# Performance work log

Measured on AMD Instinct MI355X. Metric: run time of the kernel, lower is better.

Reference implementation:

```python
import jax, jax.numpy as jnp
import numpy as np

B = 4      # cfg.TRAIN.IMS_PER_BATCH
P = 256    # proposals per image (equal per image; all labels > 0)
C = 151    # cfg.MODEL.NUM_CLASSES
R = 51     # cfg.MODEL.NUM_RELATIONS
W = 0.5    # cfg.REL_INFER.NONE_BGREL_WEIGHT


def setup_inputs() -> dict:
    key = jax.random.key(0)
    k1, k2, k3, k4 = jax.random.split(key, 4)
    roi_scores = jax.random.normal(k1, (B * P, C), dtype=jnp.float32)
    rel_scores = jax.random.normal(k2, (B * P * P, R), dtype=jnp.float32)
    roi_labels = jax.random.randint(k3, (B * P,), 1, C, dtype=jnp.int32)  # labels > 0 (fg only)
    # sparse relation co-occurrence matrix densified; background relation slice set to 1
    relationship_mat = (jax.random.uniform(k4, (C, C, R)) < 0.05).astype(jnp.float32)
    relationship_mat = relationship_mat.at[:, :, 0].set(1.0)
    return {
        "roi_scores": roi_scores,
        "rel_scores": rel_scores,
        "relationship_mat": relationship_mat,
        "roi_labels": roi_labels,
        "num_images": B,
    }


def reference(roi_scores, rel_scores, relationship_mat, roi_labels, num_images):
    nb = num_images
    p = roi_scores.shape[0] // nb
    rel = rel_scores.reshape(nb, p, p, -1)          # [B, P, P, R]
    labels = roi_labels.reshape(nb, p)              # [B, P]
    # computed in the original forward but unused by the returned loss
    _unary = jax.nn.log_softmax(roi_scores, axis=1)
    off_diag = (1.0 - jnp.eye(p, dtype=roi_scores.dtype))  # zero out p == q pairs

    def per_image(lab, rl):
        # lab: [P] int, rl: [P, P, R]
        A = relationship_mat[lab]        # [P, C, R]  rows gathered by subject label
        At = relationship_mat[:, lab]    # [C, P, R]  cols gathered by subject label
        # b[p,q,c] = A[p,c,0]*rl[p,q,0] + W * sum_{r>=1} A[p,c,r]*rl[p,q,r]
        b = A[:, None, :, 0] * rl[:, :, None, 0] \
            + W * jnp.einsum('pcr,pqr->pqc', A[..., 1:], rl[..., 1:])
        # t[p,q,c] = At[c,p,0]*rl[q,p,0] + W * sum_{r>=1} At[c,p,r]*rl[q,p,r]
        t = At[..., 0].T[:, None, :] * rl[..., 0].T[:, :, None] \
            + W * jnp.einsum('cpr,qpr->pqc', At[..., 1:], rl[..., 1:])
        theta = 0.5 * (b + t) * off_diag[:, :, None]  # mask diagonal pairs
        theta = theta.sum(0)                          # sum over partner p -> [P, C]
        logp = jax.nn.log_softmax(theta, axis=1)
        return -logp[jnp.arange(p), lab]              # [P]

    loss = jax.vmap(per_image)(labels, rel)           # [B, P]
    return loss.mean()
```

## Files before the change

kernel.cpp:

```cpp
#include <hip/hip_runtime.h>
#include <math.h>

#define NB 4
#define PP 256
#define CC 151
#define RR 51
#define CM 160
#define KS 64
#define NROW (NB*PP)
#define RELTOT (NB*PP*PP*RR)
#define ALIM (RELTOT - 8)
#define MLB 10240

typedef _Float16 half8 __attribute__((ext_vector_type(8)));
typedef float floatx16 __attribute__((ext_vector_type(16)));

#define OFF_M1 ((size_t)0)
#define OFF_M2 (OFF_M1 + (size_t)CC*MLB*2)
#define OFF_PT (OFF_M2 + (size_t)CC*MLB*2)

__global__ __launch_bounds__(256) void prep_kernel(const float* __restrict__ M,
                                                   _Float16* __restrict__ m1,
                                                   _Float16* __restrict__ m2,
                                                   float* __restrict__ out) {
    const int l = blockIdx.x;
    const int mat = blockIdx.y;
    if (l == 0 && mat == 0 && threadIdx.x == 0) *out = 0.f;
    _Float16* dst = (mat ? m2 : m1) + (size_t)l * MLB;
    for (int e = threadIdx.x; e < MLB; e += 256) {
        int oct = e / 1280;
        int rem = e - oct * 1280;
        int c = rem >> 3, j = rem & 7;
        int r = oct * 8 + j;
        float v = 0.f;
        if (r < RR && c < CC) {
            size_t src = ((size_t)(mat ? c * CC + l : l * CC + c)) * RR + r;
            v = (r == 0 ? 0.5f : 0.25f) * M[src];
        }
        dst[e] = (_Float16)v;
    }
}

__global__ __launch_bounds__(256, 2) void gemm_kernel(const float* __restrict__ rel,
                                                      const _Float16* __restrict__ m1,
                                                      const _Float16* __restrict__ m2,
                                                      const int* __restrict__ labels,
                                                      float* __restrict__ part) {
    const int tid  = threadIdx.x;
    const int ks   = blockIdx.x & 63;
    const int rbk  = (blockIdx.x >> 6) & 1;
    const int n    = blockIdx.x >> 7;
    const int wave = tid >> 6, lane = tid & 63;
    const int m32  = lane & 31, kh = lane >> 5;
    const int i0   = ks * 4;
    const int rowimg = rbk * 128 + wave * 32 + m32;

    int labs[4];
    #pragma unroll
    for (int j = 0; j < 4; ++j) labs[j] = labels[n * PP + i0 + j];

    floatx16 acc[5];
    #pragma unroll
    for (int ct = 0; ct < 5; ++ct)
        #pragma unroll
        for (int r2 = 0; r2 < 16; ++r2) acc[ct][r2] = 0.f;

    auto loadA = [&](int h, float* v) {
        const int il = h >> 3, mh = (h >> 2) & 1, t = h & 3;
        const int i = i0 + il;
        const int r0 = t * 16 + kh * 8;
        int idx = mh ? ((n * PP + rowimg) * PP + i) * RR + r0
                     : ((n * PP + i) * PP + rowimg) * RR + r0;
        idx = min(idx, ALIM);
        const float* p = rel + idx;
        #pragma unroll
        for (int j = 0; j < 8; ++j) v[j] = p[j];
    };
    auto loadB = [&](int h, half8* b) {
        const int il = h >> 3, mh = (h >> 2) & 1, t = h & 3;
        const _Float16* p = (mh ? m2 : m1) + (size_t)labs[il] * MLB + t * 2560
                          + (size_t)(kh * 160 + m32) * 8;
        #pragma unroll
        for (int ct = 0; ct < 5; ++ct) b[ct] = *(const half8*)(p + ct * 256);
    };
    auto computeStep = [&](int h, const float* av, const half8* bv) {
        const int il = h >> 3;
        const bool dz = (i0 + il) == rowimg;
        half8 a;
        #pragma unroll
        for (int j = 0; j < 8; ++j) a[j] = (_Float16)(dz ? 0.f : av[j]);
        #pragma unroll
        for (int ct = 0; ct < 5; ++ct)
            acc[ct] = __builtin_amdgcn_mfma_f32_32x32x16_f16(a, bv[ct], acc[ct], 0, 0, 0);
    };

    float aS[3][8];
    half8 bS[3][5];
    loadA(0, aS[0]); loadB(0, bS[0]);
    __builtin_amdgcn_sched_barrier(0);
    loadA(1, aS[1]); loadB(1, bS[1]);
    __builtin_amdgcn_sched_barrier(0);
    loadA(2, aS[2]); loadB(2, bS[2]);
    __builtin_amdgcn_sched_barrier(0);

    #pragma unroll
    for (int h = 0; h < 32; ++h) {
        computeStep(h, aS[h % 3], bS[h % 3]);
        if (h + 3 < 32) {
            loadA(h + 3, aS[(h + 3) % 3]);
            loadB(h + 3, bS[(h + 3) % 3]);
            __builtin_amdgcn_sched_barrier(0);
        }
    }

    float* pb = part + ((size_t)ks * NROW + n * PP + rbk * 128 + wave * 32) * CM;
    #pragma unroll
    for (int ct = 0; ct < 5; ++ct)
        #pragma unroll
        for (int reg = 0; reg < 16; ++reg) {
            int row = (reg & 3) + 8 * (reg >> 2) + 4 * kh;
            pb[(size_t)row * CM + ct * 32 + m32] = acc[ct][reg];
        }
}

__global__ __launch_bounds__(256) void reduce_loss_kernel(const float* __restrict__ part,
                                                          const int* __restrict__ labels,
                                                          float* __restrict__ out) {
    __shared__ float th[CM];
    const int row = blockIdx.x;
    const int t = threadIdx.x;
    if (t < CM) {
        float s = 0.f;
        #pragma unroll
        for (int ks = 0; ks < KS; ++ks)
            s += part[((size_t)ks * NROW + row) * CM + t];
        th[t] = s;
    }
    __syncthreads();
    if (t < 64) {
        float v0 = (t < CC)       ? th[t]       : -INFINITY;
        float v1 = (t + 64 < CC)  ? th[t + 64]  : -INFINITY;
        float v2 = (t + 128 < CC) ? th[t + 128] : -INFINITY;
        float m = fmaxf(v0, fmaxf(v1, v2));
        #pragma unroll
        for (int o = 32; o > 0; o >>= 1) m = fmaxf(m, __shfl_xor(m, o, 64));
        float s = 0.f;
        if (t < CC)       s += expf(v0 - m);
        if (t + 64 < CC)  s += expf(v1 - m);
        if (t + 128 < CC) s += expf(v2 - m);
        #pragma unroll
        for (int o = 32; o > 0; o >>= 1) s += __shfl_xor(s, o, 64);
        if (t == 0) {
            atomicAdd(out, (m + logf(s) - th[labels[row]]) * (1.0f / NROW));
        }
    }
}

extern "C" void kernel_launch(void* const* d_in, const int* in_sizes, int n_in,
                              void* d_out, int out_size, void* d_ws, size_t ws_size,
                              hipStream_t stream) {
    const float* rel    = (const float*)d_in[1];
    const float* relmat = (const float*)d_in[2];
    const int*   labels = (const int*)d_in[3];
    float* out = (float*)d_out;
    char* ws = (char*)d_ws;

    _Float16* m1 = (_Float16*)(ws + OFF_M1);
    _Float16* m2 = (_Float16*)(ws + OFF_M2);
    float*  part = (float*)(ws + OFF_PT);

    prep_kernel<<<dim3(CC, 2), 256, 0, stream>>>(relmat, m1, m2, out);
    gemm_kernel<<<NB * 2 * KS, 256, 0, stream>>>(rel, m1, m2, labels, part);
    reduce_loss_kernel<<<NROW, 256, 0, stream>>>(part, labels, out);
}
```

Baseline: 176.4 us.

## Stage relation-score tiles through LDS with coalesced vector loads and double buffering

Before this change each lane read 8 strided floats of rel_scores straight from global memory, and for the transposed half those reads were poorly coalesced. Now the block cooperatively loads each 128x51 tile with float4 loads, with consecutive threads covering one row. The tile is written into a padded, double-buffered shared-memory array, and the MFMA A operands are read back from LDS. The B-fragment prefetch is reorganised around the next tile's global loads. This adds shared memory use and a block-wide barrier per stage, which may lower occupancy and cause stalls.

After: 181.7 us. +3.0%, slower.

```diff
diff --git a/kernel.cpp b/kernel.cpp
--- a/kernel.cpp
+++ b/kernel.cpp
@@ -9,11 +9,13 @@
 #define KS 64
 #define NROW (NB*PP)
 #define RELTOT (NB*PP*PP*RR)
-#define ALIM (RELTOT - 8)
 #define MLB 10240
+#define LROW 68
 
 typedef _Float16 half8 __attribute__((ext_vector_type(8)));
 typedef float floatx16 __attribute__((ext_vector_type(16)));
+typedef float float4a __attribute__((ext_vector_type(4)));
+typedef float float4u __attribute__((ext_vector_type(4), aligned(4)));
 
 #define OFF_M1 ((size_t)0)
 #define OFF_M2 (OFF_M1 + (size_t)CC*MLB*2)
@@ -46,6 +48,7 @@
                                                       const _Float16* __restrict__ m2,
                                                       const int* __restrict__ labels,
                                                       float* __restrict__ part) {
+    __shared__ float bufA[2][128 * LROW];
     const int tid  = threadIdx.x;
     const int ks   = blockIdx.x & 63;
     const int rbk  = (blockIdx.x >> 6) & 1;
@@ -53,7 +56,8 @@
     const int wave = tid >> 6, lane = tid & 63;
     const int m32  = lane & 31, kh = lane >> 5;
     const int i0   = ks * 4;
-    const int rowimg = rbk * 128 + wave * 32 + m32;
+    const int row_loc = wave * 32 + m32;
+    const int rowimg  = rbk * 128 + row_loc;
 
     int labs[4];
     #pragma unroll
@@ -65,52 +69,86 @@
         #pragma unroll
         for (int r2 = 0; r2 < 16; ++r2) acc[ct][r2] = 0.f;
 
-    auto loadA = [&](int h, float* v) {
-        const int il = h >> 3, mh = (h >> 2) & 1, t = h & 3;
-        const int i = i0 + il;
-        const int r0 = t * 16 + kh * 8;
-        int idx = mh ? ((n * PP + rowimg) * PP + i) * RR + r0
-                     : ((n * PP + i) * PP + rowimg) * RR + r0;
-        idx = min(idx, ALIM);
-        const float* p = rel + idx;
-        #pragma unroll
-        for (int j = 0; j < 8; ++j) v[j] = p[j];
-    };
-    auto loadB = [&](int h, half8* b) {
-        const int il = h >> 3, mh = (h >> 2) & 1, t = h & 3;
-        const _Float16* p = (mh ? m2 : m1) + (size_t)labs[il] * MLB + t * 2560
-                          + (size_t)(kh * 160 + m32) * 8;
-        #pragma unroll
-        for (int ct = 0; ct < 5; ++ct) b[ct] = *(const half8*)(p + ct * 256);
-    };
-    auto computeStep = [&](int h, const float* av, const half8* bv) {
-        const int il = h >> 3;
+    const int sc  = tid & 15;
+    const int sr0 = tid >> 4;
+
+    {
+        float* z = &bufA[tid >> 7][(tid & 127) * LROW + 52];
+        float4a z4 = {0.f, 0.f, 0.f, 0.f};
+        *(float4a*)(z)      = z4;  *(float4a*)(z + 4)  = z4;
+        *(float4a*)(z + 8)  = z4;  *(float4a*)(z + 12) = z4;
+    }
+
+    auto stageLoad = [&](int p, float4u* sreg) {
+        const int il = p & 3, mt = p >> 2, i = i0 + il;
+        const size_t base = mt ? ((size_t)((n * PP + rbk * 128) * PP + i)) * RR
+                               : ((size_t)((n * PP + i) * PP + rbk * 128)) * RR;
+        const size_t stride = mt ? (size_t)PP * RR : (size_t)RR;
+        if (sc < 13) {
+            #pragma unroll
+            for (int rep = 0; rep < 8; ++rep) {
+                const float* s = rel + base + (size_t)(sr0 + rep * 16) * stride + sc * 4;
+                if (sc < 12) {
+                    sreg[rep] = *(const float4u*)s;
+                } else {
+                    float4u v; v[0] = s[0]; v[1] = s[1]; v[2] = s[2]; v[3] = 0.f;
+                    sreg[rep] = v;
+                }
+            }
+        }
+    };
+    auto stageWrite = [&](int buf, const float4u* sreg) {
+        if (sc < 13) {
+            #pragma unroll
+            for (int rep = 0; rep < 8; ++rep) {
+                float4a v = {sreg[rep][0], sreg[rep][1], sreg[rep][2], sreg[rep][3]};
+                *(float4a*)(&bufA[buf][(sr0 + rep * 16) * LROW + sc * 4]) = v;
+            }
+        }
+    };
+    auto loadB = [&](int p, int t, half8* b) {
+        const int il = p & 3, mt = p >> 2;
+        const _Float16* ptr = (mt ? m2 : m1) + (size_t)labs[il] * MLB + t * 2560
+                            + (size_t)(kh * 160 + m32) * 8;
+        #pragma unroll
+        for (int ct = 0; ct < 5; ++ct) b[ct] = *(const half8*)(ptr + ct * 256);
+    };
+    auto computeStep = [&](int p, int t, const half8* bv) {
+        const int il = p & 3, buf = p & 1;
         const bool dz = (i0 + il) == rowimg;
+        const float* ap = &bufA[buf][row_loc * LROW + t * 16 + kh * 8];
+        float4a lo = *(const float4a*)ap;
+        float4a hi = *(const float4a*)(ap + 4);
         half8 a;
         #pragma unroll
-        for (int j = 0; j < 8; ++j) a[j] = (_Float16)(dz ? 0.f : av[j]);
+        for (int j = 0; j < 4; ++j) {
+            a[j]     = (_Float16)(dz ? 0.f : lo[j]);
+            a[j + 4] = (_Float16)(dz ? 0.f : hi[j]);
+        }
         #pragma unroll
         for (int ct = 0; ct < 5; ++ct)
             acc[ct] = __builtin_amdgcn_mfma_f32_32x32x16_f16(a, bv[ct], acc[ct], 0, 0, 0);
     };
 
-    float aS[3][8];
-    half8 bS[3][5];
-    loadA(0, aS[0]); loadB(0, bS[0]);
-    __builtin_amdgcn_sched_barrier(0);
-    loadA(1, aS[1]); loadB(1, bS[1]);
-    __builtin_amdgcn_sched_barrier(0);
-    loadA(2, aS[2]); loadB(2, bS[2]);
-    __builtin_amdgcn_sched_barrier(0);
-
-    #pragma unroll
-    for (int h = 0; h < 32; ++h) {
-        computeStep(h, aS[h % 3], bS[h % 3]);
-        if (h + 3 < 32) {
-            loadA(h + 3, aS[(h + 3) % 3]);
-            loadB(h + 3, bS[(h + 3) % 3]);
-            __builtin_amdgcn_sched_barrier(0);
-        }
+    float4u sreg[8];
+    stageLoad(0, sreg);
+    stageWrite(0, sreg);
+    __syncthreads();
+
+    half8 B0[5], B1[5], B2[5], B3[5];
+    #pragma unroll
+    for (int p = 0; p < 8; ++p) {
+        loadB(p, 0, B0);
+        loadB(p, 1, B1);
+        __builtin_amdgcn_sched_barrier(0);
+        if (p < 7) stageLoad(p + 1, sreg);
+        __builtin_amdgcn_sched_barrier(0);
+        computeStep(p, 0, B0);  loadB(p, 2, B2);
+        computeStep(p, 1, B1);  loadB(p, 3, B3);
+        computeStep(p, 2, B2);
+        computeStep(p, 3, B3);
+        if (p < 7) stageWrite((p + 1) & 1, sreg);
+        __syncthreads();
     }
 
     float* pb = part + ((size_t)ks * NROW + n * PP + rbk * 128 + wave * 32) * CM;
```
